# Kernel optimization log

Hardware: AMD Instinct MI355X
Metric: run time of the kernel (lower is better)

## Reference

```python
import jax, jax.numpy as jnp
import numpy as np
from jax import lax

B, C, P = 8, 32, 256      # batch, channels, patch side
KB = 2                    # buf_region = kernel_size - stride = 3 - 1
R_MASK = 1                # output_bypassing: last-column patch, r = small_padding = 1


def setup_inputs() -> dict:
    key = jax.random.key(0)
    ks = jax.random.split(key, 5)
    x = jax.random.normal(ks[0], (B, C, P, P), jnp.float32)
    # right-halo stored by the left-neighbor patch (store_right -> last 2 cols)
    rbuf = jax.random.normal(ks[1], (B, C, P, KB), jnp.float32)
    # bottom-halo stored by the top-neighbor patch AFTER its hcat (width P+2)
    bbuf = jax.random.normal(ks[2], (B, C, KB, P + KB), jnp.float32)
    W = jax.random.normal(ks[3], (C, C, 3, 3), jnp.float32) * 0.05
    bias = jax.random.normal(ks[4], (C,), jnp.float32) * 0.05
    return {"x": x, "rbuf": rbuf, "bbuf": bbuf, "W": W, "bias": bias}


def reference(x, rbuf, bbuf, W, bias):
    # output_bypassing: zero the rightmost R_MASK columns (image right edge)
    x = x.at[:, :, :, -R_MASK:].set(0.0)
    # hcat: prepend right-halo from left neighbor -> [B,C,P,P+2]
    x = jnp.concatenate([rbuf, x], axis=-1)
    # vcat: prepend bottom-halo from top neighbor -> [B,C,P+2,P+2]
    x = jnp.concatenate([bbuf, x], axis=-2)
    # (store_bot side effect omitted: pure function returns conv output only)
    out = lax.conv_general_dilated(
        x, W, window_strides=(1, 1), padding='VALID',
        dimension_numbers=('NCHW', 'OIHW', 'NCHW'))  # -> [B,C,P,P]
    return out + bias[None, :, None, None]
```

## Files before the change

### kernel.cpp

```cpp
#include <hip/hip_runtime.h>
#include <cstdint>


constexpr int B  = 8;
constexpr int C  = 32;
constexpr int P  = 256;
constexpr int KB = 2;
constexpr int TH = 16;
constexpr int TW = 32;
constexpr int RS = 34;
constexpr int PL = 612;
constexpr int XSZ = 16 * PL;

typedef short bf16x8 __attribute__((ext_vector_type(8)));
typedef float f32x4  __attribute__((ext_vector_type(4)));
union Frag { uint32_t u[4]; bf16x8 v; };

static __device__ __forceinline__ uint32_t pk_bf16(float lo, float hi) {
    uint32_t a  = __builtin_bit_cast(uint32_t, lo);
    uint32_t b2 = __builtin_bit_cast(uint32_t, hi);
    a  += 0x7FFFu + ((a  >> 16) & 1u);
    b2 += 0x7FFFu + ((b2 >> 16) & 1u);
    return (a >> 16) | (b2 & 0xFFFF0000u);
}

__global__ __launch_bounds__(256) void pack_w_kernel(
    const float* __restrict__ W, uint32_t* __restrict__ wpk)
{
    const int g = blockIdx.x * 256 + threadIdx.x;
    const float4 v = ((const float4*)W)[g];
    const float vv[4] = { v.x, v.y, v.z, v.w };
    uint16_t* wh = (uint16_t*)wpk;
    #pragma unroll
    for (int e = 0; e < 4; ++e) {
        const int flat = 4 * g + e;
        const int t    = flat % 9;
        const int rest = flat / 9;
        const int ic   = rest & 31;
        const int oc   = rest >> 5;
        const uint32_t u = __builtin_bit_cast(uint32_t, vv[e]);
        const uint16_t h = (uint16_t)((u + 0x7FFFu + ((u >> 16) & 1u)) >> 16);
        wh[(t * 512 + oc * 16 + (ic >> 1)) * 2 + (ic & 1)] = h;
    }
}

struct StP {
    float4 a0, a1, c0, c1;
    float  h0l, h0h, h1l, h1h;
};

__global__ __launch_bounds__(256, 2) void conv_mfma(
    const float* __restrict__ x,
    const float* __restrict__ rbuf,
    const float* __restrict__ bbuf,
    const uint32_t* __restrict__ wpk,
    const float* __restrict__ bias,
    float* __restrict__ out)
{
    const int tid  = threadIdx.x;
    const int lane = tid & 63;
    const int w    = tid >> 6;
    const int q    = lane >> 4;
    const int n16  = lane & 15;

    const int sw  = (blockIdx.x & 7) * 64 + (blockIdx.x >> 3);
    const int b   = sw >> 6;
    const int ty  = (sw >> 2) & 15;
    const int cx0 = 2 * (sw & 3);
    const int x00 = cx0 * TW, x01 = x00 + TW, y0 = ty * TH;

    __shared__ uint32_t Xs[XSZ];

    const int srow = lane >> 2;
    const int scol = (lane & 3) * 8;

    int prowA[2], pcolA[2], h_ldso[2];
    #pragma unroll
    for (int ci = 0; ci < 2; ++ci) {
        const int c = lane + 64 * ci;
        int prow, pcol;
        if (c < 68) { const int hr = (c >= 34) ? 1 : 0; prow = hr; pcol = c - 34 * hr; }
        else        { const int cc = c - 68; prow = KB + (cc >> 1); pcol = cc & 1; }
        prowA[ci] = prow; pcolA[ci] = pcol;
        h_ldso[ci] = prow * RS + pcol;
    }
    const bool h1a = lane < 36;

    const float* xb = x    + (size_t)b * C * P * P;
    const float* rb = rbuf + (size_t)b * C * P * KB;
    const float* bb = bbuf + (size_t)b * C * KB * (P + KB);
    const float* basep[3] = { xb, rb, bb };
    const int    psz[3]   = { P * P, P * KB, KB * (P + KB) };

    auto mkh = [&](int x0, const float** bp, int* ps, bool* z) {
        #pragma unroll
        for (int ci = 0; ci < 2; ++ci) {
            const int gr = y0 + prowA[ci], gc = x0 + pcolA[ci];
            int sel, off; bool zz = false;
            if (gr < KB)      { sel = 2; off = gr * (P + KB) + gc; }
            else if (gc < KB) { sel = 1; off = (gr - KB) * KB + gc; }
            else              { sel = 0; off = (gr - KB) * P + (gc - KB);
                                zz = (gc == P + KB - 1); }
            bp[ci] = basep[sel] + off;
            ps[ci] = psz[sel];
            z[ci]  = zz;
        }
    };

    auto ldp = [&](int m, int x0, const float* const* bp, const int* ps,
                   const bool* z, StP& S) {
        const float* pi = xb + (size_t)(2 * m) * (P * P) + (y0 + srow) * P + x0 + scol;
        S.a0 = *(const float4*)pi;
        S.a1 = *(const float4*)(pi + 4);
        S.c0 = *(const float4*)(pi + P * P);
        S.c1 = *(const float4*)(pi + P * P + 4);
        const float* p0 = bp[0] + (size_t)(2 * m) * ps[0];
        S.h0l = z[0] ? 0.f : p0[0];
        S.h0h = z[0] ? 0.f : p0[ps[0]];
        if (h1a) {
            const float* p1 = bp[1] + (size_t)(2 * m) * ps[1];
            S.h1l = z[1] ? 0.f : p1[0];
            S.h1h = z[1] ? 0.f : p1[ps[1]];
        }
    };

    auto stp = [&](int m, const StP& S, bool zcc) {
        float4 a1 = S.a1, c1 = S.c1;
        if (zcc) { a1.w = 0.f; c1.w = 0.f; }
        uint2 p0, p1, p2, p3;
        p0.x = pk_bf16(S.a0.x, S.c0.x); p0.y = pk_bf16(S.a0.y, S.c0.y);
        p1.x = pk_bf16(S.a0.z, S.c0.z); p1.y = pk_bf16(S.a0.w, S.c0.w);
        p2.x = pk_bf16(a1.x, c1.x);     p2.y = pk_bf16(a1.y, c1.y);
        p3.x = pk_bf16(a1.z, c1.z);     p3.y = pk_bf16(a1.w, c1.w);
        uint32_t* base = Xs + m * PL + (srow + KB) * RS + KB + scol;
        *(uint2*)(base + 0) = p0;
        *(uint2*)(base + 2) = p1;
        *(uint2*)(base + 4) = p2;
        *(uint2*)(base + 6) = p3;
        Xs[m * PL + h_ldso[0]] = pk_bf16(S.h0l, S.h0h);
        if (h1a) Xs[m * PL + h_ldso[1]] = pk_bf16(S.h1l, S.h1h);
    };

    Frag Bf[9][2];
    #pragma unroll
    for (int t = 0; t < 9; ++t)
        #pragma unroll
        for (int oh = 0; oh < 2; ++oh)
            *(uint4*)Bf[t][oh].u =
                *(const uint4*)&wpk[t * 512 + (oh * 16 + n16) * 16 + q * 4];
    const float bv0 = bias[n16];
    const float bv1 = bias[16 + n16];

    auto mfma_ch = [&](int ch, int x0) {
        f32x4 acc[4][2];
        #pragma unroll
        for (int rr = 0; rr < 4; ++rr)
            #pragma unroll
            for (int oh = 0; oh < 2; ++oh)
                #pragma unroll
                for (int e = 0; e < 4; ++e) acc[rr][oh][e] = 0.f;

        #pragma unroll
        for (int dr = 0; dr < 6; ++dr) {
            Frag A[3];
            const uint32_t* ap = Xs + (4 * q) * PL + (4 * w + dr) * RS + 16 * ch + n16;
            #pragma unroll
            for (int kx = 0; kx < 3; ++kx)
                #pragma unroll
                for (int p = 0; p < 4; ++p)
                    A[kx].u[p] = ap[p * PL + kx];
            #pragma unroll
            for (int ky = 0; ky < 3; ++ky) {
                const int rr = dr - ky;
                if (rr >= 0 && rr < 4) {
                    #pragma unroll
                    for (int kx = 0; kx < 3; ++kx) {
                        acc[rr][0] = __builtin_amdgcn_mfma_f32_16x16x32_bf16(
                                         A[kx].v, Bf[ky * 3 + kx][0].v, acc[rr][0], 0, 0, 0);
                        acc[rr][1] = __builtin_amdgcn_mfma_f32_16x16x32_bf16(
                                         A[kx].v, Bf[ky * 3 + kx][1].v, acc[rr][1], 0, 0, 0);
                    }
                }
            }
        }
        #pragma unroll
        for (int oh = 0; oh < 2; ++oh) {
            const int oc = oh * 16 + n16;
            const float bv = oh ? bv1 : bv0;
            #pragma unroll
            for (int rr = 0; rr < 4; ++rr) {
                float4 v;
                v.x = acc[rr][oh][0] + bv;
                v.y = acc[rr][oh][1] + bv;
                v.z = acc[rr][oh][2] + bv;
                v.w = acc[rr][oh][3] + bv;
                *(float4*)&out[((size_t)(b * C + oc) * P + (y0 + 4 * w + rr)) * P
                               + x0 + 16 * ch + 4 * q] = v;
            }
        }
    };

    const float* bp0[2]; int ps0[2]; bool z0[2];
    mkh(x00, bp0, ps0, z0);
    StP S0[4];
    #pragma unroll
    for (int k2 = 0; k2 < 4; ++k2) ldp(4 * k2 + w, x00, bp0, ps0, z0, S0[k2]);
    #pragma unroll
    for (int k2 = 0; k2 < 4; ++k2) stp(4 * k2 + w, S0[k2], false);
    __syncthreads();

    const float* bp1[2]; int ps1[2]; bool z1[2];
    mkh(x01, bp1, ps1, z1);
    const bool zc1 = (x01 == P - TW) && ((lane & 3) == 3);
    StP S1[4];
    ldp(w,     x01, bp1, ps1, z1, S1[0]);
    ldp(4 + w, x01, bp1, ps1, z1, S1[1]);

    mfma_ch(0, x00);

    ldp(8 + w,  x01, bp1, ps1, z1, S1[2]);
    ldp(12 + w, x01, bp1, ps1, z1, S1[3]);

    mfma_ch(1, x00);
    __syncthreads();

    #pragma unroll
    for (int k2 = 0; k2 < 4; ++k2) stp(4 * k2 + w, S1[k2], zc1);
    __syncthreads();

    mfma_ch(0, x01);
    mfma_ch(1, x01);
}

extern "C" void kernel_launch(void* const* d_in, const int* in_sizes, int n_in,
                              void* d_out, int out_size, void* d_ws, size_t ws_size,
                              hipStream_t stream) {
    const float* x    = (const float*)d_in[0];
    const float* rbuf = (const float*)d_in[1];
    const float* bbuf = (const float*)d_in[2];
    const float* W    = (const float*)d_in[3];
    const float* bias = (const float*)d_in[4];
    float* out = (float*)d_out;
    uint32_t* wpk = (uint32_t*)d_ws;

    pack_w_kernel<<<9, 256, 0, stream>>>(W, wpk);
    conv_mfma<<<512, 256, 0, stream>>>(x, rbuf, bbuf, wpk, bias, out);
}
```

Baseline: 141.6 us.

## Shrink conv tiles to 16x16, stage weights in LDS, split sweeps per output half

Changes each block's work from two horizontal 16x32 tiles to two vertically stacked 16x16 tiles, which doubles the grid to 1024 blocks. Packed weights are now loaded cooperatively into shared memory and read per sweep instead of being held in 72 registers per thread. Each sweep computes one 16-channel output half, which lowers register pressure and may raise occupancy and overlap. The cost is larger halo overhead per output, more LDS traffic for re-reading weights, and narrower global loads.

```diff
diff --git a/kernel.cpp b/kernel.cpp
--- a/kernel.cpp
+++ b/kernel.cpp
@@ -6,11 +6,12 @@
 constexpr int C  = 32;
 constexpr int P  = 256;
 constexpr int KB = 2;
-constexpr int TH = 16;
-constexpr int TW = 32;
-constexpr int RS = 34;
-constexpr int PL = 612;
+constexpr int TS = 16;
+constexpr int RS = 18;
+constexpr int PL = 324;
 constexpr int XSZ = 16 * PL;
+constexpr int WOFF = XSZ;
+constexpr int LDSZ = XSZ + 4608;
 
 typedef short bf16x8 __attribute__((ext_vector_type(8)));
 typedef float f32x4  __attribute__((ext_vector_type(4)));
@@ -44,8 +45,8 @@
     }
 }
 
-struct StP {
-    float4 a0, a1, c0, c1;
+struct St16 {
+    float4 a0, c0;
     float  h0l, h0h, h1l, h1h;
 };
 
@@ -63,28 +64,30 @@
     const int q    = lane >> 4;
     const int n16  = lane & 15;
 
-    const int sw  = (blockIdx.x & 7) * 64 + (blockIdx.x >> 3);
-    const int b   = sw >> 6;
-    const int ty  = (sw >> 2) & 15;
-    const int cx0 = 2 * (sw & 3);
-    const int x00 = cx0 * TW, x01 = x00 + TW, y0 = ty * TH;
-
-    __shared__ uint32_t Xs[XSZ];
+    const int sw  = (blockIdx.x & 7) * 128 + (blockIdx.x >> 3);
+    const int b   = sw >> 7;
+    const int typ = (sw >> 4) & 7;
+    const int cx  = sw & 15;
+    const int x0  = cx * TS;
+    const int y00 = 32 * typ, y01 = y00 + 16;
+
+    __shared__ uint32_t Xs[LDSZ];
 
     const int srow = lane >> 2;
-    const int scol = (lane & 3) * 8;
+    const int scol = (lane & 3) * 4;
+    const bool zc  = (cx == 15) && ((lane & 3) == 3);
 
     int prowA[2], pcolA[2], h_ldso[2];
     #pragma unroll
     for (int ci = 0; ci < 2; ++ci) {
         const int c = lane + 64 * ci;
         int prow, pcol;
-        if (c < 68) { const int hr = (c >= 34) ? 1 : 0; prow = hr; pcol = c - 34 * hr; }
-        else        { const int cc = c - 68; prow = KB + (cc >> 1); pcol = cc & 1; }
+        if (c < 36) { const int hr = (c >= 18) ? 1 : 0; prow = hr; pcol = c - 18 * hr; }
+        else        { const int cc = c - 36; prow = KB + (cc >> 1); pcol = cc & 1; }
         prowA[ci] = prow; pcolA[ci] = pcol;
         h_ldso[ci] = prow * RS + pcol;
     }
-    const bool h1a = lane < 36;
+    const bool h1a = lane < 4;
 
     const float* xb = x    + (size_t)b * C * P * P;
     const float* rb = rbuf + (size_t)b * C * P * KB;
@@ -92,7 +95,7 @@
     const float* basep[3] = { xb, rb, bb };
     const int    psz[3]   = { P * P, P * KB, KB * (P + KB) };
 
-    auto mkh = [&](int x0, const float** bp, int* ps, bool* z) {
+    auto mkh = [&](int y0, const float** bp, int* ps, bool* z) {
         #pragma unroll
         for (int ci = 0; ci < 2; ++ci) {
             const int gr = y0 + prowA[ci], gc = x0 + pcolA[ci];
@@ -107,13 +110,11 @@
         }
     };
 
-    auto ldp = [&](int m, int x0, const float* const* bp, const int* ps,
-                   const bool* z, StP& S) {
+    auto ldp = [&](int m, int y0, const float* const* bp, const int* ps,
+                   const bool* z, St16& S) {
         const float* pi = xb + (size_t)(2 * m) * (P * P) + (y0 + srow) * P + x0 + scol;
         S.a0 = *(const float4*)pi;
-        S.a1 = *(const float4*)(pi + 4);
         S.c0 = *(const float4*)(pi + P * P);
-        S.c1 = *(const float4*)(pi + P * P + 4);
         const float* p0 = bp[0] + (size_t)(2 * m) * ps[0];
         S.h0l = z[0] ? 0.f : p0[0];
         S.h0h = z[0] ? 0.f : p0[ps[0]];
@@ -124,46 +125,37 @@
         }
     };
 
-    auto stp = [&](int m, const StP& S, bool zcc) {
-        float4 a1 = S.a1, c1 = S.c1;
-        if (zcc) { a1.w = 0.f; c1.w = 0.f; }
-        uint2 p0, p1, p2, p3;
-        p0.x = pk_bf16(S.a0.x, S.c0.x); p0.y = pk_bf16(S.a0.y, S.c0.y);
-        p1.x = pk_bf16(S.a0.z, S.c0.z); p1.y = pk_bf16(S.a0.w, S.c0.w);
-        p2.x = pk_bf16(a1.x, c1.x);     p2.y = pk_bf16(a1.y, c1.y);
-        p3.x = pk_bf16(a1.z, c1.z);     p3.y = pk_bf16(a1.w, c1.w);
+    auto stp = [&](int m, const St16& S) {
+        float4 a0 = S.a0, c0 = S.c0;
+        if (zc) { a0.w = 0.f; c0.w = 0.f; }
+        uint2 p0, p1;
+        p0.x = pk_bf16(a0.x, c0.x); p0.y = pk_bf16(a0.y, c0.y);
+        p1.x = pk_bf16(a0.z, c0.z); p1.y = pk_bf16(a0.w, c0.w);
         uint32_t* base = Xs + m * PL + (srow + KB) * RS + KB + scol;
         *(uint2*)(base + 0) = p0;
         *(uint2*)(base + 2) = p1;
-        *(uint2*)(base + 4) = p2;
-        *(uint2*)(base + 6) = p3;
         Xs[m * PL + h_ldso[0]] = pk_bf16(S.h0l, S.h0h);
         if (h1a) Xs[m * PL + h_ldso[1]] = pk_bf16(S.h1l, S.h1h);
     };
 
-    Frag Bf[9][2];
-    #pragma unroll
-    for (int t = 0; t < 9; ++t)
-        #pragma unroll
-        for (int oh = 0; oh < 2; ++oh)
-            *(uint4*)Bf[t][oh].u =
-                *(const uint4*)&wpk[t * 512 + (oh * 16 + n16) * 16 + q * 4];
-    const float bv0 = bias[n16];
-    const float bv1 = bias[16 + n16];
-
-    auto mfma_ch = [&](int ch, int x0) {
-        f32x4 acc[4][2];
+    const float bvA[2] = { bias[n16], bias[16 + n16] };
+
+    auto sweep = [&](int y0, int oh) {
+        Frag Bf[9];
+        #pragma unroll
+        for (int t = 0; t < 9; ++t)
+            *(uint4*)Bf[t].u =
+                *(const uint4*)&Xs[WOFF + t * 512 + (oh * 16 + n16) * 16 + q * 4];
+        f32x4 acc[4];
         #pragma unroll
         for (int rr = 0; rr < 4; ++rr)
             #pragma unroll
-            for (int oh = 0; oh < 2; ++oh)
-                #pragma unroll
-                for (int e = 0; e < 4; ++e) acc[rr][oh][e] = 0.f;
+            for (int e = 0; e < 4; ++e) acc[rr][e] = 0.f;
 
         #pragma unroll
         for (int dr = 0; dr < 6; ++dr) {
             Frag A[3];
-            const uint32_t* ap = Xs + (4 * q) * PL + (4 * w + dr) * RS + 16 * ch + n16;
+            const uint32_t* ap = Xs + (4 * q) * PL + (4 * w + dr) * RS + n16;
             #pragma unroll
             for (int kx = 0; kx < 3; ++kx)
                 #pragma unroll
@@ -174,62 +166,73 @@
                 const int rr = dr - ky;
                 if (rr >= 0 && rr < 4) {
                     #pragma unroll
-                    for (int kx = 0; kx < 3; ++kx) {
-                        acc[rr][0] = __builtin_amdgcn_mfma_f32_16x16x32_bf16(
-                                         A[kx].v, Bf[ky * 3 + kx][0].v, acc[rr][0], 0, 0, 0);
-                        acc[rr][1] = __builtin_amdgcn_mfma_f32_16x16x32_bf16(
-                                         A[kx].v, Bf[ky * 3 + kx][1].v, acc[rr][1], 0, 0, 0);
-                    }
+                    for (int kx = 0; kx < 3; ++kx)
+                        acc[rr] = __builtin_amdgcn_mfma_f32_16x16x32_bf16(
+                                      A[kx].v, Bf[ky * 3 + kx].v, acc[rr], 0, 0, 0);
                 }
             }
         }
-        #pragma unroll
-        for (int oh = 0; oh < 2; ++oh) {
-            const int oc = oh * 16 + n16;
-            const float bv = oh ? bv1 : bv0;
-            #pragma unroll
-            for (int rr = 0; rr < 4; ++rr) {
-                float4 v;
-                v.x = acc[rr][oh][0] + bv;
-                v.y = acc[rr][oh][1] + bv;
-                v.z = acc[rr][oh][2] + bv;
-                v.w = acc[rr][oh][3] + bv;
-                *(float4*)&out[((size_t)(b * C + oc) * P + (y0 + 4 * w + rr)) * P
-                               + x0 + 16 * ch + 4 * q] = v;
-            }
-        }
-    };
+        const int oc = oh * 16 + n16;
+        const float bv = bvA[oh];
+        #pragma unroll
+        for (int rr = 0; rr < 4; ++rr) {
+            float4 v;
+            v.x = acc[rr][0] + bv;
+            v.y = acc[rr][1] + bv;
+            v.z = acc[rr][2] + bv;
+            v.w = acc[rr][3] + bv;
+            *(float4*)&out[((size_t)(b * C + oc) * P + (y0 + 4 * w + rr)) * P
+                           + x0 + 4 * q] = v;
+        }
+    };
+
+    const uint4* wp4 = (const uint4*)wpk;
+    uint4 wv0 = wp4[tid];
+    uint4 wv1 = wp4[256 + tid];
+    uint4 wv2 = wp4[512 + tid];
+    uint4 wv3 = wp4[768 + tid];
+    uint4 wvt;
+    const bool wtail = tid < 128;
+    if (wtail) wvt = wp4[1024 + tid];
 
     const float* bp0[2]; int ps0[2]; bool z0[2];
-    mkh(x00, bp0, ps0, z0);
-    StP S0[4];
-    #pragma unroll
-    for (int k2 = 0; k2 < 4; ++k2) ldp(4 * k2 + w, x00, bp0, ps0, z0, S0[k2]);
-    #pragma unroll
-    for (int k2 = 0; k2 < 4; ++k2) stp(4 * k2 + w, S0[k2], false);
+    mkh(y00, bp0, ps0, z0);
+    St16 S0[4];
+    #pragma unroll
+    for (int k2 = 0; k2 < 4; ++k2) ldp(4 * k2 + w, y00, bp0, ps0, z0, S0[k2]);
+
+    uint4* xsW = (uint4*)(Xs + WOFF);
+    xsW[tid]       = wv0;
+    xsW[256 + tid] = wv1;
+    xsW[512 + tid] = wv2;
+    xsW[768 + tid] = wv3;
+    if (wtail) xsW[1024 + tid] = wvt;
+
+    #pragma unroll
+    for (int k2 = 0; k2 < 4; ++k2) stp(4 * k2 + w, S0[k2]);
     __syncthreads();
 
     const float* bp1[2]; int ps1[2]; bool z1[2];
-    mkh(x01, bp1, ps1, z1);
-    const bool zc1 = (x01 == P - TW) && ((lane & 3) == 3);
-    StP S1[4];
-    ldp(w,     x01, bp1, ps1, z1, S1[0]);
-    ldp(4 + w, x01, bp1, ps1, z1, S1[1]);
-
-    mfma_ch(0, x00);
-
-    ldp(8 + w,  x01, bp1, ps1, z1, S1[2]);
-    ldp(12 + w, x01, bp1, ps1, z1, S1[3]);
-
-    mfma_ch(1, x00);
+    mkh(y01, bp1, ps1, z1);
+    St16 S1[4];
+    ldp(w,     y01, bp1, ps1, z1, S1[0]);
+    ldp(4 + w, y01, bp1, ps1, z1, S1[1]);
+
+    sweep(y00, 0);
+
+    ldp(8 + w, y01, bp1, ps1, z1, S1[2]);
+
+    sweep(y00, 1);
+
+    ldp(12 + w, y01, bp1, ps1, z1, S1[3]);
     __syncthreads();
 
     #pragma unroll
-    for (int k2 = 0; k2 < 4; ++k2) stp(4 * k2 + w, S1[k2], zc1);
+    for (int k2 = 0; k2 < 4; ++k2) stp(4 * k2 + w, S1[k2]);
     __syncthreads();
 
-    mfma_ch(0, x01);
-    mfma_ch(1, x01);
+    sweep(y01, 0);
+    sweep(y01, 1);
 }
 
 extern "C" void kernel_launch(void* const* d_in, const int* in_sizes, int n_in,
@@ -244,5 +247,5 @@
     uint32_t* wpk = (uint32_t*)d_ws;
 
     pack_w_kernel<<<9, 256, 0, stream>>>(W, wpk);
-    conv_mfma<<<512, 256, 0, stream>>>(x, rbuf, bbuf, wpk, bias, out);
-}
+    conv_mfma<<<1024, 256, 0, stream>>>(x, rbuf, bbuf, wpk, bias, out);
+}
```

After: 140.7 us. Within noise of the previous version (-0.6%).
